# Performance work log

Hardware: AMD Instinct MI355X
Metric: run time of the kernel (lower is better)

The kernel has to match this reference:

```python
import jax, jax.numpy as jnp
import numpy as np

N = 30000      # nodes
E = 480000     # edges (before self-loops)
G = 30         # graphs
DIN = 256      # input_dim
DH = 64        # hidden_dim (per-head out channels)
H = 8          # heads in layers 0,1; last layer has 1 head


def _glorot(key, shape):
    fan_in, fan_out = shape[0], shape[-1]
    s = jnp.sqrt(2.0 / (fan_in + fan_out))
    return jax.random.normal(key, shape, dtype=jnp.float32) * s


def setup_inputs() -> dict:
    key = jax.random.key(0)
    ks = jax.random.split(key, 32)
    inp = {
        'x': jax.random.normal(ks[0], (N, DIN), dtype=jnp.float32),
        'edge_index': jax.random.randint(ks[1], (2, E), 0, N, dtype=jnp.int64),
        'batch': jnp.sort(jax.random.randint(ks[2], (N,), 0, G, dtype=jnp.int64)),
        # GAT layer 0: in=256 -> 8 heads x 64
        'W0': _glorot(ks[3], (DIN, H * DH)),
        'as0': _glorot(ks[4], (H, DH)), 'ad0': _glorot(ks[5], (H, DH)),
        'b0': jnp.zeros((H * DH,), jnp.float32),
        # GAT layer 1: in=512 -> 8 heads x 64
        'W1': _glorot(ks[6], (H * DH, H * DH)),
        'as1': _glorot(ks[7], (H, DH)), 'ad1': _glorot(ks[8], (H, DH)),
        'b1': jnp.zeros((H * DH,), jnp.float32),
        # GAT layer 2: in=512 -> 1 head x 64
        'W2': _glorot(ks[9], (H * DH, DH)),
        'as2': _glorot(ks[10], (1, DH)), 'ad2': _glorot(ks[11], (1, DH)),
        'b2': jnp.zeros((DH,), jnp.float32),
        # batch norms (feature sizes match actual activations)
        'bn0_g': jnp.ones((H * DH,), jnp.float32), 'bn0_b': jnp.zeros((H * DH,), jnp.float32),
        'bn1_g': jnp.ones((H * DH,), jnp.float32), 'bn1_b': jnp.zeros((H * DH,), jnp.float32),
        'bn2_g': jnp.ones((DH,), jnp.float32), 'bn2_b': jnp.zeros((DH,), jnp.float32),
        'ln_g': jnp.ones((DH,), jnp.float32), 'ln_b': jnp.zeros((DH,), jnp.float32),
        'fc1_w': _glorot(ks[12], (DH, DH // 2)), 'fc1_b': jnp.zeros((DH // 2,), jnp.float32),
        'fc2_w': _glorot(ks[13], (DH // 2, 2)), 'fc2_b': jnp.zeros((2,), jnp.float32),
    }
    return inp


def _gat(x, src, dst, W, a_src, a_dst, bias, heads):
    # x: [N, Fin]; project to [N, heads, DH]
    h = (x @ W).reshape(N, heads, DH)
    s_src = jnp.sum(h * a_src, axis=-1)  # [N, heads]
    s_dst = jnp.sum(h * a_dst, axis=-1)  # [N, heads]
    e = jax.nn.leaky_relu(s_src[src] + s_dst[dst], 0.2)  # [Etot, heads]
    # segment softmax over edges grouped by destination node
    m = jax.ops.segment_max(e, dst, num_segments=N)
    p = jnp.exp(e - m[dst])
    denom = jax.ops.segment_sum(p, dst, num_segments=N)
    alpha = p / (denom[dst] + 1e-16)
    out = jax.ops.segment_sum(h[src] * alpha[:, :, None], dst, num_segments=N)
    return out.reshape(N, heads * DH) + bias


def _bn(x, g, b):
    m = jnp.mean(x, axis=0)
    v = jnp.var(x, axis=0)
    return (x - m) / jnp.sqrt(v + 1e-5) * g + b


def _forward(x, edge_index, batch,
             W0, as0, ad0, b0, W1, as1, ad1, b1, W2, as2, ad2, b2,
             bn0_g, bn0_b, bn1_g, bn1_b, bn2_g, bn2_b,
             ln_g, ln_b, fc1_w, fc1_b, fc2_w, fc2_b):
    loops = jnp.arange(N, dtype=edge_index.dtype)
    src = jnp.concatenate([edge_index[0], loops])
    dst = jnp.concatenate([edge_index[1], loops])
    # layer 0: 256 -> 512; no residual (dim mismatch)
    x1 = jax.nn.elu(_bn(_gat(x, src, dst, W0, as0, ad0, b0, H), bn0_g, bn0_b))
    # layer 1: 512 -> 512; residual
    x2 = jax.nn.elu(_bn(_gat(x1, src, dst, W1, as1, ad1, b1, H), bn1_g, bn1_b)) + x1
    # layer 2 (single head): 512 -> 64; no residual
    x3 = jax.nn.elu(_bn(_gat(x2, src, dst, W2, as2, ad2, b2, 1), bn2_g, bn2_b))
    # layer norm
    mu = jnp.mean(x3, axis=-1, keepdims=True)
    var = jnp.var(x3, axis=-1, keepdims=True)
    xl = (x3 - mu) / jnp.sqrt(var + 1e-5) * ln_g + ln_b
    # global mean pool over graphs
    sums = jax.ops.segment_sum(xl, batch, num_segments=G)
    cnt = jax.ops.segment_sum(jnp.ones((N, 1), xl.dtype), batch, num_segments=G)
    pooled = sums / jnp.maximum(cnt, 1.0)
    hdd = jax.nn.elu(pooled @ fc1_w + fc1_b)
    logits = hdd @ fc2_w + fc2_b
    return jax.nn.log_softmax(logits, axis=1)


def reference(x, edge_index, batch,
              W0, as0, ad0, b0, W1, as1, ad1, b1, W2, as2, ad2, b2,
              bn0_g, bn0_b, bn1_g, bn1_b, bn2_g, bn2_b,
              ln_g, ln_b, fc1_w, fc1_b, fc2_w, fc2_b):
    return _forward(x, edge_index, batch,
                    W0, as0, ad0, b0, W1, as1, ad1, b1, W2, as2, ad2, b2,
                    bn0_g, bn0_b, bn1_g, bn1_b, bn2_g, bn2_b,
                    ln_g, ln_b, fc1_w, fc1_b, fc2_w, fc2_b)
```

## Files before the change

kernel.cpp:

```cpp
#include <hip/hip_runtime.h>
#include <math.h>

#define NODES 30000
#define NEDGE 480000
#define ETOT  (NODES + NEDGE)
#define NGRAPH 30
#define DIN 256
#define DH 64
#define CAP 128

typedef __bf16 bf16x8 __attribute__((ext_vector_type(8)));
typedef float  f32x4  __attribute__((ext_vector_type(4)));

static __device__ __forceinline__ float elu_f(float x){ return x > 0.f ? x : expm1f(x); }
static __device__ __forceinline__ float bf_lo(unsigned v){ return __uint_as_float(v << 16); }
static __device__ __forceinline__ float bf_hi(unsigned v){ return __uint_as_float(v & 0xffff0000u); }
static __device__ __forceinline__ unsigned pack_bf2(float a, float b){
  __bf16 ob[2] = {(__bf16)a, (__bf16)b};
  return *(unsigned*)ob;
}

__global__ void k_count(const int* __restrict__ ei, int* __restrict__ deg){
  int e = blockIdx.x*256 + threadIdx.x;
  if (e >= ETOT) return;
  int dst = (e < NEDGE) ? ei[NEDGE + e] : (e - NEDGE);
  atomicAdd(&deg[dst], 1);
}

__global__ void k_scan(const int* __restrict__ deg, int* __restrict__ rowptr){
  __shared__ int s[1024];
  int t = threadIdx.x;
  const int CH = (NODES + 1023) / 1024;
  int base = t * CH;
  int local = 0;
  for (int i = 0; i < CH; i++){ int idx = base + i; if (idx < NODES) local += deg[idx]; }
  s[t] = local; __syncthreads();
  for (int off = 1; off < 1024; off <<= 1){
    int v = (t >= off) ? s[t - off] : 0;
    __syncthreads();
    s[t] += v;
    __syncthreads();
  }
  int run = s[t] - local;
  for (int i = 0; i < CH; i++){
    int idx = base + i;
    if (idx < NODES){ rowptr[idx] = run; run += deg[idx]; }
  }
  if (t == 1023) rowptr[NODES] = s[1023];
}

__global__ void k_fill(const int* __restrict__ ei, const int* __restrict__ rowptr,
                       int* __restrict__ cursor, int* __restrict__ colA){
  int e = blockIdx.x*256 + threadIdx.x;
  if (e >= ETOT) return;
  int src, dst;
  if (e < NEDGE){ src = ei[e]; dst = ei[NEDGE + e]; }
  else          { src = e - NEDGE; dst = src; }
  int pos = atomicAdd(&cursor[dst], 1);
  colA[rowptr[dst] + pos] = src;
}

__global__ void k_cast4(const float* __restrict__ in, __bf16* __restrict__ out, int n4){
  int i = blockIdx.x*256 + threadIdx.x;
  if (i >= n4) return;
  float4 v = ((const float4*)in)[i];
  __bf16 o[4] = {(__bf16)v.x, (__bf16)v.y, (__bf16)v.z, (__bf16)v.w};
  *(uint2*)(out + (size_t)i*4) = *(const uint2*)o;
}

#define TW0 (512*256)
#define TW1 (512*512)
#define TW2 (64*512)
__global__ void k_transW_all(const float* __restrict__ W0, const float* __restrict__ W1,
                             const float* __restrict__ W2, __bf16* __restrict__ Wt0,
                             __bf16* __restrict__ Wt1, __bf16* __restrict__ Wt2){
  int idx = blockIdx.x*256 + threadIdx.x;
  if (idx < TW0){
    int n = idx >> 8, k = idx & 255;
    Wt0[idx] = (__bf16)W0[(size_t)k*512 + n];
  } else if (idx < TW0 + TW1){
    int j = idx - TW0;
    int n = j >> 9, k = j & 511;
    Wt1[j] = (__bf16)W1[(size_t)k*512 + n];
  } else if (idx < TW0 + TW1 + TW2){
    int j = idx - TW0 - TW1;
    int n = j >> 9, k = j & 511;
    Wt2[j] = (__bf16)W2[(size_t)k*64 + n];
  }
}

#define LSTR 72
__global__ __launch_bounds__(256) void k_gemm_bf16(const __bf16* __restrict__ A,
    const __bf16* __restrict__ Bt, __bf16* __restrict__ C,
    const float* __restrict__ asrc, const float* __restrict__ adst,
    float* __restrict__ ssrc, float* __restrict__ sdst, int heads,
    int M, int N, int K){
  __shared__ __align__(16) __bf16 As[128*LSTR];
  __shared__ __align__(16) __bf16 Bs[128*LSTR];
  int tid  = threadIdx.x;
  int lane = tid & 63, wave = tid >> 6;
  int wr = wave >> 1, wc = wave & 1;
  int q = lane >> 4, r = lane & 15;
  int rowBase = blockIdx.y * 128, colBase = blockIdx.x * 128;
  f32x4 acc[4][4] = {};
  for (int k0 = 0; k0 < K; k0 += 64){
    #pragma unroll
    for (int p = 0; p < 4; p++){
      int lin = p*256 + tid;
      int rr = lin >> 3, ko = (lin & 7) * 8;
      uint4 va = make_uint4(0,0,0,0);
      int gr = rowBase + rr;
      if (gr < M) va = *(const uint4*)(A + (size_t)gr*K + k0 + ko);
      *(uint4*)(&As[rr*LSTR + ko]) = va;
      uint4 vb = make_uint4(0,0,0,0);
      int gn = colBase + rr;
      if (gn < N) vb = *(const uint4*)(Bt + (size_t)gn*K + k0 + ko);
      *(uint4*)(&Bs[rr*LSTR + ko]) = vb;
    }
    __syncthreads();
    #pragma unroll
    for (int kk = 0; kk < 2; kk++){
      bf16x8 af[4], bfr[4];
      #pragma unroll
      for (int i = 0; i < 4; i++) af[i]  = *(const bf16x8*)(&As[(wr*64 + i*16 + r)*LSTR + kk*32 + q*8]);
      #pragma unroll
      for (int j = 0; j < 4; j++) bfr[j] = *(const bf16x8*)(&Bs[(wc*64 + j*16 + r)*LSTR + kk*32 + q*8]);
      #pragma unroll
      for (int i = 0; i < 4; i++)
        #pragma unroll
        for (int j = 0; j < 4; j++)
          acc[i][j] = __builtin_amdgcn_mfma_f32_16x16x32_bf16(af[i], bfr[j], acc[i][j], 0, 0, 0);
    }
    __syncthreads();
  }
  #pragma unroll
  for (int i = 0; i < 4; i++){
    #pragma unroll
    for (int j = 0; j < 4; j++){
      int col = colBase + wc*64 + j*16 + r;
      if (col >= N) continue;
      #pragma unroll
      for (int v = 0; v < 4; v++){
        int row = rowBase + wr*64 + i*16 + q*4 + v;
        if (row < M) C[(size_t)row*N + col] = (__bf16)acc[i][j][v];
      }
    }
  }
  int colW = colBase + wc*64;
  if (colW < N){
    int hb = colW >> 6;
    float a_s[4], a_d[4];
    #pragma unroll
    for (int j = 0; j < 4; j++){
      a_s[j] = asrc[hb*64 + j*16 + r];
      a_d[j] = adst[hb*64 + j*16 + r];
    }
    #pragma unroll
    for (int i = 0; i < 4; i++){
      #pragma unroll
      for (int v = 0; v < 4; v++){
        float s1 = 0.f, s2 = 0.f;
        #pragma unroll
        for (int j = 0; j < 4; j++){
          float av = acc[i][j][v];
          s1 += av * a_s[j];
          s2 += av * a_d[j];
        }
        #pragma unroll
        for (int off = 1; off < 16; off <<= 1){
          s1 += __shfl_xor(s1, off, 64);
          s2 += __shfl_xor(s2, off, 64);
        }
        if (r == 0){
          int row = rowBase + wr*64 + i*16 + q*4 + v;
          if (row < M){
            ssrc[(size_t)row*heads + hb] = s1;
            sdst[(size_t)row*heads + hb] = s2;
          }
        }
      }
    }
  }
}

__global__ __launch_bounds__(256) void k_gatagg8(const __bf16* __restrict__ hb,
    const float* __restrict__ ssrc, const float* __restrict__ sdst,
    const int* __restrict__ rowptr, const int* __restrict__ colA,
    const float* __restrict__ bias, __bf16* __restrict__ outb){
  int n = blockIdx.x;
  int t = threadIdx.x;
  __shared__ int ecol[CAP];
  __shared__ float p[CAP][9];
  __shared__ float dhv[8], sdsh[8], mh[8];
  int base = rowptr[n];
  int deg = rowptr[n+1] - base;
  if (t < 8) sdsh[t] = sdst[(size_t)n*8 + t];
  __syncthreads();
  int g = t >> 5, l = t & 31;
  if (deg <= CAP){
    if (t < deg){
      int c = colA[base + t];
      ecol[t] = c;
      const float4* sp = (const float4*)(ssrc + (size_t)c*8);
      float4 s0 = sp[0], s1 = sp[1];
      float v;
      v = s0.x + sdsh[0]; p[t][0] = v > 0.f ? v : 0.2f*v;
      v = s0.y + sdsh[1]; p[t][1] = v > 0.f ? v : 0.2f*v;
      v = s0.z + sdsh[2]; p[t][2] = v > 0.f ? v : 0.2f*v;
      v = s0.w + sdsh[3]; p[t][3] = v > 0.f ? v : 0.2f*v;
      v = s1.x + sdsh[4]; p[t][4] = v > 0.f ? v : 0.2f*v;
      v = s1.y + sdsh[5]; p[t][5] = v > 0.f ? v : 0.2f*v;
      v = s1.z + sdsh[6]; p[t][6] = v > 0.f ? v : 0.2f*v;
      v = s1.w + sdsh[7]; p[t][7] = v > 0.f ? v : 0.2f*v;
    }
    __syncthreads();
    {
      float m = -1e30f;
      for (int e = l; e < deg; e += 32) m = fmaxf(m, p[e][g]);
      #pragma unroll
      for (int off = 1; off < 32; off <<= 1) m = fmaxf(m, __shfl_xor(m, off, 64));
      float d = 0.f;
      for (int e = l; e < deg; e += 32){ float xv = __expf(p[e][g] - m); p[e][g] = xv; d += xv; }
      #pragma unroll
      for (int off = 1; off < 32; off <<= 1) d += __shfl_xor(d, off, 64);
      if (l == 0) dhv[g] = 1.f / (d + 1e-16f);
    }
    __syncthreads();
    int hh = g;
    float rcp = dhv[hh];
    float a0 = 0.f, a1 = 0.f, b0 = 0.f, b1 = 0.f;
    int e = 0;
    for (; e + 4 <= deg; e += 4){
      int c0 = ecol[e], c1 = ecol[e+1], c2 = ecol[e+2], c3 = ecol[e+3];
      float p0 = p[e][hh], p1 = p[e+1][hh], p2 = p[e+2][hh], p3 = p[e+3][hh];
      unsigned v0 = *(const unsigned*)(hb + (size_t)c0*512 + t*2);
      unsigned v1 = *(const unsigned*)(hb + (size_t)c1*512 + t*2);
      unsigned v2 = *(const unsigned*)(hb + (size_t)c2*512 + t*2);
      unsigned v3 = *(const unsigned*)(hb + (size_t)c3*512 + t*2);
      a0 += p0*bf_lo(v0); a1 += p0*bf_hi(v0);
      b0 += p1*bf_lo(v1); b1 += p1*bf_hi(v1);
      a0 += p2*bf_lo(v2); a1 += p2*bf_hi(v2);
      b0 += p3*bf_lo(v3); b1 += p3*bf_hi(v3);
    }
    for (; e < deg; e++){
      int c = ecol[e];
      float pe = p[e][hh];
      unsigned v = *(const unsigned*)(hb + (size_t)c*512 + t*2);
      a0 += pe*bf_lo(v); a1 += pe*bf_hi(v);
    }
    a0 += b0; a1 += b1;
    float o0 = a0*rcp + bias[t*2], o1 = a1*rcp + bias[t*2+1];
    *(unsigned*)(outb + (size_t)n*512 + t*2) = pack_bf2(o0, o1);
  } else {
    float m = -1e30f;
    for (int e = l; e < deg; e += 32){
      int c = colA[base + e];
      float sc = ssrc[(size_t)c*8 + g] + sdsh[g];
      sc = sc > 0.f ? sc : 0.2f*sc;
      m = fmaxf(m, sc);
    }
    #pragma unroll
    for (int off = 1; off < 32; off <<= 1) m = fmaxf(m, __shfl_xor(m, off, 64));
    if (l == 0) mh[g] = m;
    __syncthreads();
    float d = 0.f;
    float mm = mh[g];
    for (int e = l; e < deg; e += 32){
      int c = colA[base + e];
      float sc = ssrc[(size_t)c*8 + g] + sdsh[g];
      sc = sc > 0.f ? sc : 0.2f*sc;
      d += __expf(sc - mm);
    }
    #pragma unroll
    for (int off = 1; off < 32; off <<= 1) d += __shfl_xor(d, off, 64);
    if (l == 0) dhv[g] = 1.f / (d + 1e-16f);
    __syncthreads();
    int hh = g;
    float rcp = dhv[hh];
    float mhh = mh[hh];
    float a0 = 0.f, a1 = 0.f;
    for (int e = 0; e < deg; e++){
      int c = colA[base + e];
      float sc = ssrc[(size_t)c*8 + hh] + sdsh[hh];
      sc = sc > 0.f ? sc : 0.2f*sc;
      float pe = __expf(sc - mhh);
      unsigned v = *(const unsigned*)(hb + (size_t)c*512 + t*2);
      a0 += pe*bf_lo(v); a1 += pe*bf_hi(v);
    }
    float o0 = a0*rcp + bias[t*2], o1 = a1*rcp + bias[t*2+1];
    *(unsigned*)(outb + (size_t)n*512 + t*2) = pack_bf2(o0, o1);
  }
}

__global__ __launch_bounds__(256) void k_gatagg1(const __bf16* __restrict__ hb,
    const float* __restrict__ ssrc, const float* __restrict__ sdst,
    const int* __restrict__ rowptr, const int* __restrict__ colA,
    const float* __restrict__ bias, __bf16* __restrict__ outb){
  int n = blockIdx.x;
  int t = threadIdx.x;
  __shared__ int ecol[CAP];
  __shared__ float p[CAP];
  __shared__ float racc[8][64];
  __shared__ float dhv1, mh1, sds;
  int base = rowptr[n];
  int deg = rowptr[n+1] - base;
  if (t == 0) sds = sdst[n];
  __syncthreads();
  int g = t >> 5, l = t & 31;
  if (deg <= CAP){
    if (t < deg){
      int c = colA[base + t];
      ecol[t] = c;
      float sc = ssrc[c] + sds;
      p[t] = sc > 0.f ? sc : 0.2f*sc;
    }
    __syncthreads();
    if (t < 64){
      float m = -1e30f;
      for (int e = t; e < deg; e += 64) m = fmaxf(m, p[e]);
      #pragma unroll
      for (int off = 1; off < 64; off <<= 1) m = fmaxf(m, __shfl_xor(m, off, 64));
      float d = 0.f;
      for (int e = t; e < deg; e += 64){ float xv = __expf(p[e] - m); p[e] = xv; d += xv; }
      #pragma unroll
      for (int off = 1; off < 64; off <<= 1) d += __shfl_xor(d, off, 64);
      if (t == 0) dhv1 = 1.f / (d + 1e-16f);
    }
    __syncthreads();
    float a0 = 0.f, a1 = 0.f;
    for (int e = g; e < deg; e += 8){
      float pe = p[e];
      unsigned v = *(const unsigned*)(hb + (size_t)ecol[e]*64 + l*2);
      a0 += pe*bf_lo(v); a1 += pe*bf_hi(v);
    }
    racc[g][l*2] = a0; racc[g][l*2+1] = a1;
    __syncthreads();
    if (t < 32){
      float s0 = 0.f, s1 = 0.f;
      #pragma unroll
      for (int g2 = 0; g2 < 8; g2++){ s0 += racc[g2][t*2]; s1 += racc[g2][t*2+1]; }
      float rcp = dhv1;
      float o0 = s0*rcp + bias[t*2], o1 = s1*rcp + bias[t*2+1];
      *(unsigned*)(outb + (size_t)n*64 + t*2) = pack_bf2(o0, o1);
    }
  } else {
    if (t < 64){
      float m = -1e30f;
      for (int e = t; e < deg; e += 64){
        int c = colA[base + e];
        float sc = ssrc[c] + sds;
        sc = sc > 0.f ? sc : 0.2f*sc;
        m = fmaxf(m, sc);
      }
      #pragma unroll
      for (int off = 1; off < 64; off <<= 1) m = fmaxf(m, __shfl_xor(m, off, 64));
      if (t == 0) mh1 = m;
    }
    __syncthreads();
    if (t < 64){
      float d = 0.f;
      for (int e = t; e < deg; e += 64){
        int c = colA[base + e];
        float sc = ssrc[c] + sds;
        sc = sc > 0.f ? sc : 0.2f*sc;
        d += __expf(sc - mh1);
      }
      #pragma unroll
      for (int off = 1; off < 64; off <<= 1) d += __shfl_xor(d, off, 64);
      if (t == 0) dhv1 = 1.f / (d + 1e-16f);
    }
    __syncthreads();
    float a0 = 0.f, a1 = 0.f;
    float mm = mh1;
    for (int e = g; e < deg; e += 8){
      int c = colA[base + e];
      float sc = ssrc[c] + sds;
      sc = sc > 0.f ? sc : 0.2f*sc;
      float pe = __expf(sc - mm);
      unsigned v = *(const unsigned*)(hb + (size_t)c*64 + l*2);
      a0 += pe*bf_lo(v); a1 += pe*bf_hi(v);
    }
    racc[g][l*2] = a0; racc[g][l*2+1] = a1;
    __syncthreads();
    if (t < 32){
      float s0 = 0.f, s1 = 0.f;
      #pragma unroll
      for (int g2 = 0; g2 < 8; g2++){ s0 += racc[g2][t*2]; s1 += racc[g2][t*2+1]; }
      float rcp = dhv1;
      float o0 = s0*rcp + bias[t*2], o1 = s1*rcp + bias[t*2+1];
      *(unsigned*)(outb + (size_t)n*64 + t*2) = pack_bf2(o0, o1);
    }
  }
}

__global__ __launch_bounds__(256) void k_bnstat1(const __bf16* __restrict__ xb,
    float* __restrict__ partial, int F){
  int t = threadIdx.x;
  int OCT = F >> 3;
  int RPB = 256 / OCT;
  int o = t & (OCT - 1), r = t / OCT;
  int NB = gridDim.x;
  float s[8] = {}, q[8] = {};
  int step = NB * RPB;
  for (int n = blockIdx.x*RPB + r; n < NODES; n += step){
    uint4 v = *(const uint4*)(xb + (size_t)n*F + o*8);
    unsigned vv[4] = {v.x, v.y, v.z, v.w};
    #pragma unroll
    for (int j = 0; j < 4; j++){
      float lo = bf_lo(vv[j]), hi = bf_hi(vv[j]);
      s[2*j]   += lo; q[2*j]   += lo*lo;
      s[2*j+1] += hi; q[2*j+1] += hi*hi;
    }
  }
  __shared__ float red[256][17];
  #pragma unroll
  for (int j = 0; j < 8; j++){ red[t][j] = s[j]; red[t][8+j] = q[j]; }
  __syncthreads();
  for (int st = RPB >> 1; st > 0; st >>= 1){
    if (r < st){
      #pragma unroll
      for (int j = 0; j < 16; j++) red[t][j] += red[t + st*OCT][j];
    }
    __syncthreads();
  }
  if (r == 0){
    #pragma unroll
    for (int j = 0; j < 8; j++){
      partial[(size_t)(o*8 + j)*NB + blockIdx.x]     = red[t][j];
      partial[(size_t)(F + o*8 + j)*NB + blockIdx.x] = red[t][8 + j];
    }
  }
}

__global__ void k_bnstat2(const float* __restrict__ partial, float* __restrict__ sum,
                          float* __restrict__ sumsq, int F, int NB){
  int row = blockIdx.x;
  int t = threadIdx.x;
  float a = 0.f;
  for (int i = t; i < NB; i += 64) a += partial[(size_t)row*NB + i];
  #pragma unroll
  for (int off = 1; off < 64; off <<= 1) a += __shfl_xor(a, off, 64);
  if (t == 0){
    if (row < F) sum[row] = a;
    else         sumsq[row - F] = a;
  }
}

__global__ __launch_bounds__(256) void k_bnapply_b(const __bf16* __restrict__ xb,
    const float* __restrict__ sum, const float* __restrict__ sumsq,
    const float* __restrict__ g, const float* __restrict__ b,
    const __bf16* __restrict__ res, __bf16* __restrict__ y, int rows){
  int t = threadIdx.x;
  float2 sm = *(const float2*)(sum + t*2);
  float2 sq = *(const float2*)(sumsq + t*2);
  float2 gg = *(const float2*)(g + t*2);
  float2 bb = *(const float2*)(b + t*2);
  const float inv_n = 1.f / (float)NODES;
  float m0 = sm.x*inv_n, m1 = sm.y*inv_n;
  float v0 = sq.x*inv_n - m0*m0, v1 = sq.y*inv_n - m1*m1;
  float sc0 = gg.x * rsqrtf(v0 + 1e-5f), sc1 = gg.y * rsqrtf(v1 + 1e-5f);
  float sh0 = bb.x - m0*sc0, sh1 = bb.y - m1*sc1;
  int n0 = blockIdx.x * rows;
  for (int r = 0; r < rows; r++){
    int n = n0 + r;
    if (n >= NODES) break;
    size_t off = (size_t)n*512 + t*2;
    unsigned v = *(const unsigned*)(xb + off);
    float o0 = elu_f(bf_lo(v)*sc0 + sh0);
    float o1 = elu_f(bf_hi(v)*sc1 + sh1);
    if (res){
      unsigned rv = *(const unsigned*)(res + off);
      o0 += bf_lo(rv); o1 += bf_hi(rv);
    }
    *(unsigned*)(y + off) = pack_bf2(o0, o1);
  }
}

__global__ void k_bn_elu_ln_b(const __bf16* __restrict__ xb, const float* __restrict__ sum,
    const float* __restrict__ sumsq, const float* __restrict__ g, const float* __restrict__ b,
    const float* __restrict__ lg, const float* __restrict__ lb, float* __restrict__ y){
  int t = threadIdx.x;
  int l = t & 31, sub = t >> 5;
  int n = blockIdx.x*8 + sub;
  float2 sm = *(const float2*)(sum + l*2);
  float2 sq = *(const float2*)(sumsq + l*2);
  float2 gg = *(const float2*)(g + l*2);
  float2 bb = *(const float2*)(b + l*2);
  const float inv_n = 1.f / (float)NODES;
  float m0 = sm.x*inv_n, m1 = sm.y*inv_n;
  float va0 = sq.x*inv_n - m0*m0, va1 = sq.y*inv_n - m1*m1;
  float sc0 = gg.x * rsqrtf(va0 + 1e-5f), sc1 = gg.y * rsqrtf(va1 + 1e-5f);
  float sh0 = bb.x - m0*sc0, sh1 = bb.y - m1*sc1;
  unsigned v = *(const unsigned*)(xb + (size_t)n*64 + l*2);
  float x0 = elu_f(bf_lo(v)*sc0 + sh0);
  float x1 = elu_f(bf_hi(v)*sc1 + sh1);
  float s = x0 + x1;
  #pragma unroll
  for (int off = 1; off < 32; off <<= 1) s += __shfl_xor(s, off, 64);
  float mean = s * (1.f/64.f);
  float d0 = x0 - mean, d1 = x1 - mean;
  float qq = d0*d0 + d1*d1;
  #pragma unroll
  for (int off = 1; off < 32; off <<= 1) qq += __shfl_xor(qq, off, 64);
  float var = qq * (1.f/64.f);
  float inv = rsqrtf(var + 1e-5f);
  float2 o = make_float2(d0*inv*lg[l*2] + lb[l*2], d1*inv*lg[l*2+1] + lb[l*2+1]);
  *(float2*)(y + (size_t)n*64 + l*2) = o;
}

static __device__ int lbound(const int* a, int n, int v){
  int lo = 0, hi = n;
  while (lo < hi){ int mid = (lo + hi) >> 1; if (a[mid] < v) lo = mid + 1; else hi = mid; }
  return lo;
}

__global__ void k_pool(const float* __restrict__ xl, const int* __restrict__ batch,
                       float* __restrict__ pooled){
  int g = blockIdx.x;
  int t = threadIdx.x;
  int lo = lbound(batch, NODES, g);
  int hi = lbound(batch, NODES, g+1);
  int f = t & 63, grp = t >> 6;
  float acc = 0.f;
  for (int n = lo + grp; n < hi; n += 4) acc += xl[(size_t)n*DH + f];
  __shared__ float red[4][64];
  red[grp][f] = acc;
  __syncthreads();
  if (grp == 0){
    float s = red[0][f] + red[1][f] + red[2][f] + red[3][f];
    int cnt = hi - lo;
    pooled[g*DH + f] = s / fmaxf((float)cnt, 1.f);
  }
}

__global__ void k_head(const float* __restrict__ pooled, const float* __restrict__ w1,
                       const float* __restrict__ b1, const float* __restrict__ w2,
                       const float* __restrict__ b2, float* __restrict__ out){
  int g = threadIdx.x;
  if (g >= NGRAPH) return;
  const float* pd = pooled + g*DH;
  float hdd[32];
  for (int j = 0; j < 32; j++){
    float s = b1[j];
    for (int d = 0; d < DH; d++) s += pd[d]*w1[d*32 + j];
    hdd[j] = elu_f(s);
  }
  float l0 = b2[0], l1 = b2[1];
  for (int j = 0; j < 32; j++){ l0 += hdd[j]*w2[j*2]; l1 += hdd[j]*w2[j*2 + 1]; }
  float m = fmaxf(l0, l1);
  float lse = m + logf(expf(l0 - m) + expf(l1 - m));
  out[g*2]     = l0 - lse;
  out[g*2 + 1] = l1 - lse;
}

extern "C" void kernel_launch(void* const* d_in, const int* in_sizes, int n_in,
                              void* d_out, int out_size, void* d_ws, size_t ws_size,
                              hipStream_t stream){
  const float* x    = (const float*)d_in[0];
  const int*   ei   = (const int*)d_in[1];
  const int*   batch= (const int*)d_in[2];
  const float* W0   = (const float*)d_in[3];
  const float* as0  = (const float*)d_in[4];
  const float* ad0  = (const float*)d_in[5];
  const float* b0   = (const float*)d_in[6];
  const float* W1   = (const float*)d_in[7];
  const float* as1  = (const float*)d_in[8];
  const float* ad1  = (const float*)d_in[9];
  const float* b1   = (const float*)d_in[10];
  const float* W2   = (const float*)d_in[11];
  const float* as2  = (const float*)d_in[12];
  const float* ad2  = (const float*)d_in[13];
  const float* b2   = (const float*)d_in[14];
  const float* bn0g = (const float*)d_in[15];
  const float* bn0b = (const float*)d_in[16];
  const float* bn1g = (const float*)d_in[17];
  const float* bn1b = (const float*)d_in[18];
  const float* bn2g = (const float*)d_in[19];
  const float* bn2b = (const float*)d_in[20];
  const float* lng  = (const float*)d_in[21];
  const float* lnb  = (const float*)d_in[22];
  const float* fc1w = (const float*)d_in[23];
  const float* fc1b = (const float*)d_in[24];
  const float* fc2w = (const float*)d_in[25];
  const float* fc2b = (const float*)d_in[26];
  float* out = (float*)d_out;

  char* w = (char*)d_ws;
  auto alloc = [&](size_t bytes) -> char* {
    char* p = w; w += (bytes + 255) & ~(size_t)255; return p;
  };
  __bf16* xb0   = (__bf16*)alloc((size_t)NODES*DIN*2);
  __bf16* hbuf  = (__bf16*)alloc((size_t)NODES*512*2);
  __bf16* gbuf  = (__bf16*)alloc((size_t)NODES*512*2);
  __bf16* x1b   = (__bf16*)alloc((size_t)NODES*512*2);
  __bf16* x2b   = (__bf16*)alloc((size_t)NODES*512*2);
  __bf16* Wt0   = (__bf16*)alloc((size_t)TW0*2);
  __bf16* Wt1   = (__bf16*)alloc((size_t)TW1*2);
  __bf16* Wt2   = (__bf16*)alloc((size_t)TW2*2);
  float*  ssrc  = (float*)alloc((size_t)NODES*8*4);
  float*  sdst  = (float*)alloc((size_t)NODES*8*4);
  float*  xl    = (float*)alloc((size_t)NODES*DH*4);
  float*  pooled= (float*)alloc(NGRAPH*DH*4);
  int*    rowptr= (int*)alloc((NODES+1)*4);
  int*    colA  = (int*)alloc((size_t)ETOT*4);
  float*  partial=(float*)alloc((size_t)2*512*512*4);
  float*  sum0  = (float*)alloc(512*4);
  float*  sq0   = (float*)alloc(512*4);
  float*  sum1  = (float*)alloc(512*4);
  float*  sq1   = (float*)alloc(512*4);
  float*  sum2  = (float*)alloc(64*4);
  float*  sq2   = (float*)alloc(64*4);
  char* zbase  = w;
  int*   deg   = (int*)alloc(NODES*4);
  int*   cursor= (int*)alloc(NODES*4);
  size_t zbytes = (size_t)(w - zbase);
  hipMemsetAsync(zbase, 0, zbytes, stream);

  const int eb = (ETOT + 255)/256;
  k_count<<<eb, 256, 0, stream>>>(ei, deg);
  k_scan<<<1, 1024, 0, stream>>>(deg, rowptr);
  k_fill<<<eb, 256, 0, stream>>>(ei, rowptr, cursor, colA);

  k_cast4<<<(NODES*DIN/4 + 255)/256, 256, 0, stream>>>(x, xb0, NODES*DIN/4);
  k_transW_all<<<(TW0+TW1+TW2 + 255)/256, 256, 0, stream>>>(W0, W1, W2, Wt0, Wt1, Wt2);

  const int mb128 = (NODES + 127)/128;
  const int nb8 = (NODES + 7)/8;

  k_gemm_bf16<<<dim3(4, mb128), 256, 0, stream>>>(xb0, Wt0, hbuf, as0, ad0, ssrc, sdst, 8, NODES, 512, DIN);
  k_gatagg8<<<NODES, 256, 0, stream>>>(hbuf, ssrc, sdst, rowptr, colA, b0, gbuf);
  k_bnstat1<<<512, 256, 0, stream>>>(gbuf, partial, 512);
  k_bnstat2<<<1024, 64, 0, stream>>>(partial, sum0, sq0, 512, 512);
  k_bnapply_b<<<nb8, 256, 0, stream>>>(gbuf, sum0, sq0, bn0g, bn0b, nullptr, x1b, 8);

  k_gemm_bf16<<<dim3(4, mb128), 256, 0, stream>>>(x1b, Wt1, hbuf, as1, ad1, ssrc, sdst, 8, NODES, 512, 512);
  k_gatagg8<<<NODES, 256, 0, stream>>>(hbuf, ssrc, sdst, rowptr, colA, b1, gbuf);
  k_bnstat1<<<512, 256, 0, stream>>>(gbuf, partial, 512);
  k_bnstat2<<<1024, 64, 0, stream>>>(partial, sum1, sq1, 512, 512);
  k_bnapply_b<<<nb8, 256, 0, stream>>>(gbuf, sum1, sq1, bn1g, bn1b, x1b, x2b, 8);

  k_gemm_bf16<<<dim3(1, mb128), 256, 0, stream>>>(x2b, Wt2, hbuf, as2, ad2, ssrc, sdst, 1, NODES, 64, 512);
  k_gatagg1<<<NODES, 256, 0, stream>>>(hbuf, ssrc, sdst, rowptr, colA, b2, gbuf);
  k_bnstat1<<<256, 256, 0, stream>>>(gbuf, partial, 64);
  k_bnstat2<<<128, 64, 0, stream>>>(partial, sum2, sq2, 64, 256);
  k_bn_elu_ln_b<<<nb8, 256, 0, stream>>>(gbuf, sum2, sq2, bn2g, bn2b, lng, lnb, xl);

  k_pool<<<NGRAPH, 256, 0, stream>>>(xl, batch, pooled);
  k_head<<<1, 32, 0, stream>>>(pooled, fc1w, fc1b, fc2w, fc2b, out);
}
```

Measured before the change: 750.6 us.

## Split 8-head GAT aggregation into per-edge alpha and column-sliced gather kernels

Replaces the fused per-node 8-head aggregation kernel with two kernels. One computes normalized softmax attention weights per edge and head into a head-major buffer. The other gathers features with one block per 8 nodes and one 64-column head slice, so each block touches only one head's slice of the source rows for better cache locality. This adds an 8*ETOT float write and read per layer and one more launch. The x cast and weight transpose kernels are also merged into a single prep launch.

```diff
diff --git a/kernel.cpp b/kernel.cpp
--- a/kernel.cpp
+++ b/kernel.cpp
@@ -60,32 +60,33 @@
   colA[rowptr[dst] + pos] = src;
 }
 
-__global__ void k_cast4(const float* __restrict__ in, __bf16* __restrict__ out, int n4){
-  int i = blockIdx.x*256 + threadIdx.x;
-  if (i >= n4) return;
-  float4 v = ((const float4*)in)[i];
-  __bf16 o[4] = {(__bf16)v.x, (__bf16)v.y, (__bf16)v.z, (__bf16)v.w};
-  *(uint2*)(out + (size_t)i*4) = *(const uint2*)o;
-}
-
+#define NCAST4 (NODES*DIN/4)
 #define TW0 (512*256)
 #define TW1 (512*512)
 #define TW2 (64*512)
-__global__ void k_transW_all(const float* __restrict__ W0, const float* __restrict__ W1,
-                             const float* __restrict__ W2, __bf16* __restrict__ Wt0,
-                             __bf16* __restrict__ Wt1, __bf16* __restrict__ Wt2){
+__global__ void k_prep(const float* __restrict__ x, __bf16* __restrict__ xb0,
+                       const float* __restrict__ W0, const float* __restrict__ W1,
+                       const float* __restrict__ W2, __bf16* __restrict__ Wt0,
+                       __bf16* __restrict__ Wt1, __bf16* __restrict__ Wt2){
   int idx = blockIdx.x*256 + threadIdx.x;
-  if (idx < TW0){
-    int n = idx >> 8, k = idx & 255;
-    Wt0[idx] = (__bf16)W0[(size_t)k*512 + n];
-  } else if (idx < TW0 + TW1){
-    int j = idx - TW0;
-    int n = j >> 9, k = j & 511;
-    Wt1[j] = (__bf16)W1[(size_t)k*512 + n];
-  } else if (idx < TW0 + TW1 + TW2){
-    int j = idx - TW0 - TW1;
-    int n = j >> 9, k = j & 511;
-    Wt2[j] = (__bf16)W2[(size_t)k*64 + n];
+  if (idx < NCAST4){
+    float4 v = ((const float4*)x)[idx];
+    __bf16 o[4] = {(__bf16)v.x, (__bf16)v.y, (__bf16)v.z, (__bf16)v.w};
+    *(uint2*)(xb0 + (size_t)idx*4) = *(const uint2*)o;
+    return;
+  }
+  int j = idx - NCAST4;
+  if (j < TW0){
+    int n = j >> 8, k = j & 255;
+    Wt0[j] = (__bf16)W0[(size_t)k*512 + n];
+  } else if (j < TW0 + TW1){
+    int j1 = j - TW0;
+    int n = j1 >> 9, k = j1 & 511;
+    Wt1[j1] = (__bf16)W1[(size_t)k*512 + n];
+  } else if (j < TW0 + TW1 + TW2){
+    int j2 = j - TW0 - TW1;
+    int n = j2 >> 9, k = j2 & 511;
+    Wt2[j2] = (__bf16)W2[(size_t)k*64 + n];
   }
 }
 
@@ -183,13 +184,11 @@
   }
 }
 
-__global__ __launch_bounds__(256) void k_gatagg8(const __bf16* __restrict__ hb,
-    const float* __restrict__ ssrc, const float* __restrict__ sdst,
-    const int* __restrict__ rowptr, const int* __restrict__ colA,
-    const float* __restrict__ bias, __bf16* __restrict__ outb){
+__global__ __launch_bounds__(256) void k_alpha8(const float* __restrict__ ssrc,
+    const float* __restrict__ sdst, const int* __restrict__ rowptr,
+    const int* __restrict__ colA, float* __restrict__ ealpha){
   int n = blockIdx.x;
   int t = threadIdx.x;
-  __shared__ int ecol[CAP];
   __shared__ float p[CAP][9];
   __shared__ float dhv[8], sdsh[8], mh[8];
   int base = rowptr[n];
@@ -200,7 +199,6 @@
   if (deg <= CAP){
     if (t < deg){
       int c = colA[base + t];
-      ecol[t] = c;
       const float4* sp = (const float4*)(ssrc + (size_t)c*8);
       float4 s0 = sp[0], s1 = sp[1];
       float v;
@@ -226,31 +224,11 @@
       if (l == 0) dhv[g] = 1.f / (d + 1e-16f);
     }
     __syncthreads();
-    int hh = g;
-    float rcp = dhv[hh];
-    float a0 = 0.f, a1 = 0.f, b0 = 0.f, b1 = 0.f;
-    int e = 0;
-    for (; e + 4 <= deg; e += 4){
-      int c0 = ecol[e], c1 = ecol[e+1], c2 = ecol[e+2], c3 = ecol[e+3];
-      float p0 = p[e][hh], p1 = p[e+1][hh], p2 = p[e+2][hh], p3 = p[e+3][hh];
-      unsigned v0 = *(const unsigned*)(hb + (size_t)c0*512 + t*2);
-      unsigned v1 = *(const unsigned*)(hb + (size_t)c1*512 + t*2);
-      unsigned v2 = *(const unsigned*)(hb + (size_t)c2*512 + t*2);
-      unsigned v3 = *(const unsigned*)(hb + (size_t)c3*512 + t*2);
-      a0 += p0*bf_lo(v0); a1 += p0*bf_hi(v0);
-      b0 += p1*bf_lo(v1); b1 += p1*bf_hi(v1);
-      a0 += p2*bf_lo(v2); a1 += p2*bf_hi(v2);
-      b0 += p3*bf_lo(v3); b1 += p3*bf_hi(v3);
-    }
-    for (; e < deg; e++){
-      int c = ecol[e];
-      float pe = p[e][hh];
-      unsigned v = *(const unsigned*)(hb + (size_t)c*512 + t*2);
-      a0 += pe*bf_lo(v); a1 += pe*bf_hi(v);
-    }
-    a0 += b0; a1 += b1;
-    float o0 = a0*rcp + bias[t*2], o1 = a1*rcp + bias[t*2+1];
-    *(unsigned*)(outb + (size_t)n*512 + t*2) = pack_bf2(o0, o1);
+    if (t < deg){
+      #pragma unroll
+      for (int h = 0; h < 8; h++)
+        ealpha[(size_t)h*ETOT + base + t] = p[t][h] * dhv[h];
+    }
   } else {
     float m = -1e30f;
     for (int e = l; e < deg; e += 32){
@@ -275,21 +253,75 @@
     for (int off = 1; off < 32; off <<= 1) d += __shfl_xor(d, off, 64);
     if (l == 0) dhv[g] = 1.f / (d + 1e-16f);
     __syncthreads();
-    int hh = g;
-    float rcp = dhv[hh];
-    float mhh = mh[hh];
-    float a0 = 0.f, a1 = 0.f;
+    for (int e = t; e < deg; e += 256){
+      int c = colA[base + e];
+      const float4* sp = (const float4*)(ssrc + (size_t)c*8);
+      float4 s0 = sp[0], s1 = sp[1];
+      float sc[8] = {s0.x, s0.y, s0.z, s0.w, s1.x, s1.y, s1.z, s1.w};
+      #pragma unroll
+      for (int h = 0; h < 8; h++){
+        float v = sc[h] + sdsh[h];
+        v = v > 0.f ? v : 0.2f*v;
+        ealpha[(size_t)h*ETOT + base + e] = __expf(v - mh[h]) * dhv[h];
+      }
+    }
+  }
+}
+
+__global__ __launch_bounds__(256) void k_gather8(const __bf16* __restrict__ hb,
+    const float* __restrict__ ealpha, const int* __restrict__ rowptr,
+    const int* __restrict__ colA, const float* __restrict__ bias,
+    __bf16* __restrict__ outb){
+  int cs = blockIdx.x;
+  int t = threadIdx.x;
+  int sub = t >> 5, l = t & 31;
+  int n = blockIdx.y*8 + sub;
+  __shared__ int   ecol[8][CAP];
+  __shared__ float ealf[8][CAP];
+  int base = rowptr[n];
+  int deg = rowptr[n+1] - base;
+  const float* ap = ealpha + (size_t)cs*ETOT;
+  int degc = min(deg, CAP);
+  for (int e = l; e < degc; e += 32){
+    ecol[sub][e] = __builtin_nontemporal_load(&colA[base + e]);
+    ealf[sub][e] = __builtin_nontemporal_load(&ap[base + e]);
+  }
+  __syncthreads();
+  int fo = cs*64 + l*2;
+  float a0 = 0.f, a1 = 0.f, b0 = 0.f, b1 = 0.f;
+  if (deg <= CAP){
+    int e = 0;
+    for (; e + 4 <= deg; e += 4){
+      int c0 = ecol[sub][e],   c1 = ecol[sub][e+1];
+      int c2 = ecol[sub][e+2], c3 = ecol[sub][e+3];
+      float p0 = ealf[sub][e],   p1 = ealf[sub][e+1];
+      float p2 = ealf[sub][e+2], p3 = ealf[sub][e+3];
+      unsigned v0 = *(const unsigned*)(hb + (size_t)c0*512 + fo);
+      unsigned v1 = *(const unsigned*)(hb + (size_t)c1*512 + fo);
+      unsigned v2 = *(const unsigned*)(hb + (size_t)c2*512 + fo);
+      unsigned v3 = *(const unsigned*)(hb + (size_t)c3*512 + fo);
+      a0 += p0*bf_lo(v0); a1 += p0*bf_hi(v0);
+      b0 += p1*bf_lo(v1); b1 += p1*bf_hi(v1);
+      a0 += p2*bf_lo(v2); a1 += p2*bf_hi(v2);
+      b0 += p3*bf_lo(v3); b1 += p3*bf_hi(v3);
+    }
+    for (; e < deg; e++){
+      int c = ecol[sub][e];
+      float pe = ealf[sub][e];
+      unsigned v = *(const unsigned*)(hb + (size_t)c*512 + fo);
+      a0 += pe*bf_lo(v); a1 += pe*bf_hi(v);
+    }
+    a0 += b0; a1 += b1;
+  } else {
     for (int e = 0; e < deg; e++){
-      int c = colA[base + e];
-      float sc = ssrc[(size_t)c*8 + hh] + sdsh[hh];
-      sc = sc > 0.f ? sc : 0.2f*sc;
-      float pe = __expf(sc - mhh);
-      unsigned v = *(const unsigned*)(hb + (size_t)c*512 + t*2);
+      int c = __builtin_nontemporal_load(&colA[base + e]);
+      float pe = __builtin_nontemporal_load(&ap[base + e]);
+      unsigned v = *(const unsigned*)(hb + (size_t)c*512 + fo);
       a0 += pe*bf_lo(v); a1 += pe*bf_hi(v);
     }
-    float o0 = a0*rcp + bias[t*2], o1 = a1*rcp + bias[t*2+1];
-    *(unsigned*)(outb + (size_t)n*512 + t*2) = pack_bf2(o0, o1);
-  }
+  }
+  float o0 = a0 + bias[fo], o1 = a1 + bias[fo + 1];
+  *(unsigned*)(outb + (size_t)n*512 + fo) = pack_bf2(o0, o1);
 }
 
 __global__ __launch_bounds__(256) void k_gatagg1(const __bf16* __restrict__ hb,
@@ -599,6 +631,7 @@
   __bf16* Wt2   = (__bf16*)alloc((size_t)TW2*2);
   float*  ssrc  = (float*)alloc((size_t)NODES*8*4);
   float*  sdst  = (float*)alloc((size_t)NODES*8*4);
+  float*  ealpha= (float*)alloc((size_t)8*ETOT*4);
   float*  xl    = (float*)alloc((size_t)NODES*DH*4);
   float*  pooled= (float*)alloc(NGRAPH*DH*4);
   int*    rowptr= (int*)alloc((NODES+1)*4);
@@ -621,20 +654,23 @@
   k_scan<<<1, 1024, 0, stream>>>(deg, rowptr);
   k_fill<<<eb, 256, 0, stream>>>(ei, rowptr, cursor, colA);
 
-  k_cast4<<<(NODES*DIN/4 + 255)/256, 256, 0, stream>>>(x, xb0, NODES*DIN/4);
-  k_transW_all<<<(TW0+TW1+TW2 + 255)/256, 256, 0, stream>>>(W0, W1, W2, Wt0, Wt1, Wt2);
+  const int prep_total = NCAST4 + TW0 + TW1 + TW2;
+  k_prep<<<(prep_total + 255)/256, 256, 0, stream>>>(x, xb0, W0, W1, W2, Wt0, Wt1, Wt2);
 
   const int mb128 = (NODES + 127)/128;
   const int nb8 = (NODES + 7)/8;
+  const dim3 ggrid(8, NODES/8);
 
   k_gemm_bf16<<<dim3(4, mb128), 256, 0, stream>>>(xb0, Wt0, hbuf, as0, ad0, ssrc, sdst, 8, NODES, 512, DIN);
-  k_gatagg8<<<NODES, 256, 0, stream>>>(hbuf, ssrc, sdst, rowptr, colA, b0, gbuf);
+  k_alpha8<<<NODES, 256, 0, stream>>>(ssrc, sdst, rowptr, colA, ealpha);
+  k_gather8<<<ggrid, 256, 0, stream>>>(hbuf, ealpha, rowptr, colA, b0, gbuf);
   k_bnstat1<<<512, 256, 0, stream>>>(gbuf, partial, 512);
   k_bnstat2<<<1024, 64, 0, stream>>>(partial, sum0, sq0, 512, 512);
   k_bnapply_b<<<nb8, 256, 0, stream>>>(gbuf, sum0, sq0, bn0g, bn0b, nullptr, x1b, 8);
 
   k_gemm_bf16<<<dim3(4, mb128), 256, 0, stream>>>(x1b, Wt1, hbuf, as1, ad1, ssrc, sdst, 8, NODES, 512, 512);
-  k_gatagg8<<<NODES, 256, 0, stream>>>(hbuf, ssrc, sdst, rowptr, colA, b1, gbuf);
+  k_alpha8<<<NODES, 256, 0, stream>>>(ssrc, sdst, rowptr, colA, ealpha);
+  k_gather8<<<ggrid, 256, 0, stream>>>(hbuf, ealpha, rowptr, colA, b1, gbuf);
   k_bnstat1<<<512, 256, 0, stream>>>(gbuf, partial, 512);
   k_bnstat2<<<1024, 64, 0, stream>>>(partial, sum1, sq1, 512, 512);
   k_bnapply_b<<<nb8, 256, 0, stream>>>(gbuf, sum1, sq1, bn1g, bn1b, x1b, x2b, 8);
```

After: 790.3 us. +5.3%, slower.
